# Kernel tuning notes

Measured on AMD Instinct MI355X. Metric: run time of the kernel, lower is better.

## Reference

```python
import jax, jax.numpy as jnp
from jax import lax
import numpy as np

VOCAB, EMB, HID, ENC, ATT, P = 10000, 512, 1024, 2048, 512, 196
B, T = 64, 160
PAD_IDX = 3

def setup_inputs() -> dict:
    key = jax.random.key(0)
    ks = jax.random.split(key, 20)
    s = 0.02
    emb = jax.random.normal(ks[0], (VOCAB, EMB), jnp.float32) * s
    emb = emb.at[PAD_IDX].set(0.0)
    return {
        'image_embedding': jax.random.normal(ks[1], (B, P, ENC), jnp.float32),
        'padded_sentence': jax.random.randint(ks[2], (B, T), 0, VOCAB),
        'enc_h': jax.random.normal(ks[3], (2, B, HID // 2), jnp.float32),
        'enc_c': jax.random.normal(ks[4], (2, B, HID // 2), jnp.float32),
        'sentence_lens': jax.random.randint(ks[5], (B,), 1, T + 1),
        'emb': emb,
        'Wea': jax.random.normal(ks[6], (ATT, ENC), jnp.float32) * s,
        'bea': jnp.zeros((ATT,), jnp.float32),
        'Wda': jax.random.normal(ks[7], (ATT, HID), jnp.float32) * s,
        'bda': jnp.zeros((ATT,), jnp.float32),
        'wfa': jax.random.normal(ks[8], (ATT,), jnp.float32) * s,
        'bfa': jnp.zeros((), jnp.float32),
        'Wfb': jax.random.normal(ks[9], (ENC, HID), jnp.float32) * s,
        'bfb': jnp.zeros((ENC,), jnp.float32),
        'Wih': jax.random.normal(ks[10], (4 * HID, EMB + ENC), jnp.float32) * s,
        'bih': jnp.zeros((4 * HID,), jnp.float32),
        'Whh': jax.random.normal(ks[11], (4 * HID, HID), jnp.float32) * s,
        'bhh': jnp.zeros((4 * HID,), jnp.float32),
    }


def reference(image_embedding, padded_sentence, enc_h, enc_c, sentence_lens,
              emb, Wea, bea, Wda, bda, wfa, bfa, Wfb, bfb, Wih, bih, Whh, bhh):
    Tn = padded_sentence.shape[1]
    # sort by descending length (replicates sentence_lens.sort(descending=True))
    idx = jnp.argsort(-sentence_lens)
    img = image_embedding[idx]                   # [B,P,E]
    sent = padded_sentence[idx]                  # [B,T]
    lens = sentence_lens[idx]                    # [B]
    h0 = jnp.concatenate([enc_h[-2], enc_h[-1]], axis=1)[idx]  # [B,HID]
    c0 = jnp.concatenate([enc_c[-2], enc_c[-1]], axis=1)[idx]
    emb_eff = emb.at[PAD_IDX].set(0.0)           # padding_idx=3
    x_emb = emb_eff[sent]                        # [B,T,EMB]
    # encoder projection is h-independent: hoist out of the scan
    att1 = jnp.einsum('bpe,ae->bpa', img, Wea) + bea  # [B,P,ATT]

    def step(carry, xt):
        h, c = carry
        x_t, t = xt
        active = (t < lens)[:, None]             # ragged mask
        att2 = h @ Wda.T + bda                   # [B,ATT]
        e = jax.nn.relu(att1 + att2[:, None, :]) @ wfa + bfa  # [B,P]
        alpha = jax.nn.softmax(e, axis=1)
        context = jnp.einsum('bp,bpe->be', alpha, img)        # [B,ENC]
        gate = jax.nn.sigmoid(h @ Wfb.T + bfb)
        inp = jnp.concatenate([x_t, gate * context], axis=1)  # [B,EMB+ENC]
        gates = inp @ Wih.T + bih + h @ Whh.T + bhh           # [B,4*HID]
        i, f, g, o = jnp.split(gates, 4, axis=1)
        c_new = jax.nn.sigmoid(f) * c + jax.nn.sigmoid(i) * jnp.tanh(g)
        h_new = jax.nn.sigmoid(o) * jnp.tanh(c_new)
        h = jnp.where(active, h_new, h)
        c = jnp.where(active, c_new, c)
        out_t = jnp.where(active, h_new, 0.0)
        alpha_t = jnp.where(active, alpha, 0.0)
        return (h, c), (out_t, alpha_t)

    (_, _), (outs, alphas) = lax.scan(
        step, (h0, c0), (jnp.swapaxes(x_emb, 0, 1), jnp.arange(Tn)))
    outputs = jnp.swapaxes(outs, 0, 1)           # [B,T,HID]
    alphas = jnp.swapaxes(alphas, 0, 1)          # [B,T,P]
    # replicate the original's final reindex (outputs[ordered_idx], not inverse)
    return outputs[idx], alphas[idx]
```

## Files before the change

### kernel.cpp

```cpp
#include <hip/hip_runtime.h>
#include <hip/hip_bf16.h>
#include <math.h>

#define B 64
#define T 160
#define P 196
#define ENC 2048
#define ATT 512
#define EMB 512
#define HID 1024
#define KTOT 3584
#define N2 2560
#define KT4 112
#define NTHR 1024
#define NBLK 256
#define NGRP 16
#define GRPSZ (NBLK/NGRP)

typedef __attribute__((ext_vector_type(8))) short bf16x8;
typedef __attribute__((ext_vector_type(4))) float f32x4;
typedef float __attribute__((ext_vector_type(4))) vf4;

__device__ __forceinline__ float sigm(float x){ return 1.0f/(1.0f+__expf(-x)); }
__device__ __forceinline__ float bfu(short s){ return __uint_as_float(((unsigned)(unsigned short)s) << 16); }

__device__ __forceinline__ float ldgf(const float* p){ return *(const volatile float*)p; }
__device__ __forceinline__ void stgf(float* p, float v){ *(volatile float*)p = v; }
__device__ __forceinline__ void stgu(unsigned* p, unsigned v){ *(volatile unsigned*)p = v; }
__device__ __forceinline__ unsigned pkbf(float a, float b){
    unsigned ua = (unsigned)__bfloat16_as_ushort(__float2bfloat16(a));
    unsigned ub = (unsigned)__bfloat16_as_ushort(__float2bfloat16(b));
    return ua | (ub << 16);
}

__device__ __forceinline__ void gbar_arrive(unsigned* bar, unsigned k){
    asm volatile("s_waitcnt vmcnt(0)" ::: "memory");
    __syncthreads();
    if (threadIdx.x == 0){
        unsigned g = blockIdx.x & (NGRP-1);
        unsigned old = __hip_atomic_fetch_add(bar + g*256, 1u, __ATOMIC_RELAXED, __HIP_MEMORY_SCOPE_AGENT);
        if (old == (k + 1u)*GRPSZ - 1u){
            __hip_atomic_fetch_add(bar + NGRP*256, 1u, __ATOMIC_RELAXED, __HIP_MEMORY_SCOPE_AGENT);
        }
    }
}
__device__ __forceinline__ void gbar_wait(unsigned* bar, unsigned k){
    if (threadIdx.x == 0){
        unsigned b = blockIdx.x;
        if (b < NGRP){
            volatile unsigned* top = bar + NGRP*256;
            while (*top < (k + 1u)*NGRP) __builtin_amdgcn_s_sleep(2);
            *(volatile unsigned*)(bar + (NGRP + 1 + b)*256) = k + 1u;
        } else {
            volatile unsigned* rel = bar + (NGRP + 1 + (b & (NGRP-1)))*256;
            while (*rel < k + 1u) __builtin_amdgcn_s_sleep(2);
        }
    }
    __syncthreads();
    asm volatile("" ::: "memory");
}
__device__ __forceinline__ void gbar(unsigned* bar, unsigned k){
    gbar_arrive(bar, k);
    gbar_wait(bar, k);
}

__global__ void k_sort(const int* lens, int* idx, int* rank, unsigned* barCnt, int* nAct){
    __shared__ int L[B];
    int i = threadIdx.x;
    L[i] = lens[i];
    if (i < 33) barCnt[i*256] = 0u;
    __syncthreads();
    int li = L[i];
    int r = 0;
    for (int j = 0; j < B; ++j){
        int lj = L[j];
        if (lj > li || (lj == li && j < i)) r++;
    }
    rank[i] = r;
    idx[r] = i;
    for (int tt = i; tt < T; tt += B){
        int c = 0;
        for (int j = 0; j < B; ++j) c += (L[j] > tt) ? 1 : 0;
        nAct[tt] = c;
    }
}

__global__ void k_init_hc(const float* enc_h, const float* enc_c, const int* idx,
                          float* h, float* c, __hip_bfloat16* hbR0){
    int j = blockIdx.x;
    int o = idx[j];
    for (int k = threadIdx.x; k < HID; k += blockDim.x){
        float hv = (k < 512) ? enc_h[o*512 + k] : enc_h[B*512 + o*512 + (k-512)];
        float cv = (k < 512) ? enc_c[o*512 + k] : enc_c[B*512 + o*512 + (k-512)];
        h[j*HID + k] = hv;
        c[j*HID + k] = cv;
        hbR0[j*HID + k] = __float2bfloat16(hv);
    }
}

__global__ void k_cvt_wcat(const float* Wih, const float* Whh, __hip_bfloat16* Wfrag){
    size_t i = (size_t)blockIdx.x*256 + threadIdx.x;
    int e = (int)(i & 7);
    size_t t2 = i >> 3;
    int lane = (int)(t2 & 63);
    size_t t3 = t2 >> 6;
    int kt = (int)(t3 % KT4);
    int strip = (int)(t3 / KT4);
    int n = strip*16 + (lane & 15);
    int r = (n & 3)*HID + (n >> 2);
    int k = kt*32 + (lane >> 4)*8 + e;
    float v = (k < EMB+ENC) ? Wih[(size_t)r*(EMB+ENC) + k]
                            : Whh[(size_t)r*HID + (k - EMB - ENC)];
    Wfrag[i] = __float2bfloat16(v);
}

__global__ void k_bsum(const float* bih, const float* bhh, float* bsum){
    int n = blockIdx.x*256 + threadIdx.x;
    int r = (n & 3)*HID + (n >> 2);
    bsum[n] = bih[r] + bhh[r];
}

__global__ void k_cvt_w2(const float* Wda, const float* bda, const float* Wfb, const float* bfb,
                         __hip_bfloat16* W2, float* bias2){
    int n = blockIdx.x;
    const float* src = (n < ATT) ? (Wda + (size_t)n*HID) : (Wfb + (size_t)(n-ATT)*HID);
    __hip_bfloat16* dst = W2 + (size_t)n*HID;
    for (int k = threadIdx.x; k < HID; k += 256) dst[k] = __float2bfloat16(src[k]);
    if (threadIdx.x == 0) bias2[n] = (n < ATT) ? bda[n] : bfb[n-ATT];
}

__global__ void k_cvt_emb(const float* emb, __hip_bfloat16* emb_bf){
    size_t i = (size_t)blockIdx.x*256 + threadIdx.x;
    emb_bf[i] = __float2bfloat16(emb[i]);
}

__global__ void k_cvt_wea(const float* Wea, __hip_bfloat16* Wea_bf){
    int n = blockIdx.x;
    for (int k = threadIdx.x; k < ENC; k += 256)
        Wea_bf[(size_t)n*ENC + k] = __float2bfloat16(Wea[(size_t)n*ENC + k]);
}

__global__ void k_cvt_img(const float* img, const int* idx, __hip_bfloat16* img_s){
    int j = blockIdx.y;
    int o = idx[j];
    size_t off = (size_t)blockIdx.x*256 + threadIdx.x;
    img_s[(size_t)j*P*ENC + off] = __float2bfloat16(img[(size_t)o*P*ENC + off]);
}

__global__ __launch_bounds__(256) void k_att1m(const __hip_bfloat16* img_s, const __hip_bfloat16* Wea_bf,
                                               const float* bea, __hip_bfloat16* att1w){
    int m0 = blockIdx.x * 64, n0 = blockIdx.y * 64;
    int tid = threadIdx.x, w = tid >> 6, l = tid & 63, lm = l & 15, lk = l >> 4;
    const short* ap = (const short*)img_s + (size_t)(m0 + 16*w + lm)*ENC + 8*lk;
    const short* bp = (const short*)Wea_bf + (size_t)(n0 + lm)*ENC + 8*lk;
    f32x4 acc[4];
    #pragma unroll
    for (int nt=0; nt<4; ++nt) acc[nt] = (f32x4){0.f,0.f,0.f,0.f};
    #pragma unroll 4
    for (int kt = 0; kt < ENC/32; ++kt){
        bf16x8 a = *(const bf16x8*)(ap + kt*32);
        #pragma unroll
        for (int nt=0; nt<4; ++nt){
            bf16x8 bb = *(const bf16x8*)(bp + (size_t)nt*16*ENC + kt*32);
            acc[nt] = __builtin_amdgcn_mfma_f32_16x16x32_bf16(a, bb, acc[nt], 0,0,0);
        }
    }
    #pragma unroll
    for (int nt=0; nt<4; ++nt){
        int n = n0 + nt*16 + lm;
        float bv = bea[n];
        #pragma unroll
        for (int r=0; r<4; ++r){
            int m = m0 + 16*w + 4*lk + r;
            att1w[(size_t)m*ATT + n] = __float2bfloat16(acc[nt][r] + bv);
        }
    }
}

struct SP {
    const __hip_bfloat16 *att1w, *img_s, *emb_bf, *Wfrag, *W2;
    const float *bsum, *bias2, *wfa, *bfa;
    const int *sent, *idx, *rank, *lens, *nAct;
    float *D2;
    __hip_bfloat16 *gcR, *hbR;
    float *hF0, *hF1, *cW;
    float *outH, *outA;
    unsigned *barCnt;
};

__global__ __launch_bounds__(1024, 4) void k_scan(SP p){
    __shared__ short WcatL[KT4*64*8];
    __shared__ union {
        struct { float Dp[4][64][17]; float hS[64][4]; int tokL[64], lensL[64], wLs[64]; } gem;
        struct { float att2L[512]; float wfaL[512]; float red[1024]; float aL[208]; float ctxP[8][512]; } p23;
    } sh;

    int b = blockIdx.x, tid = threadIdx.x;
    int w = tid >> 6, l = tid & 63, lm = l & 15, lk = l >> 4;
    unsigned bk = 0;

    {
        const bf16x8* src = (const bf16x8*)((const short*)p.Wfrag + (size_t)b*KT4*64*8);
        bf16x8* dst = (bf16x8*)WcatL;
        #pragma unroll
        for (int i = 0; i < KT4*64/NTHR; ++i) dst[tid + i*NTHR] = src[tid + i*NTHR];
    }
    __syncthreads();

    float bfa0 = p.bfa[0];

    for (int t = 0; t < T; ++t){
        const __hip_bfloat16* hbIn = p.hbR + (size_t)t*B*HID;
        __hip_bfloat16*       hbOut = p.hbR + (size_t)(t+1)*B*HID;
        const __hip_bfloat16* gcT  = p.gcR + (size_t)t*B*ENC;
        const float* hFIn = (t & 1) ? p.hF1 : p.hF0;
        float*       hFOut = (t & 1) ? p.hF0 : p.hF1;
        int nAct = p.nAct[t];

        if (b < N2/16){
            int n0 = b*16;
            int rt = w & 3, kq = w >> 2;
            if (16*rt < nAct){
                const short* ap = (const short*)hbIn + (size_t)(16*rt + lm)*HID + kq*256 + 8*lk;
                const short* bp = (const short*)p.W2 + (size_t)(n0 + lm)*HID + kq*256 + 8*lk;
                f32x4 acc = {0.f,0.f,0.f,0.f};
                #pragma unroll
                for (int kt = 0; kt < 8; ++kt){
                    bf16x8 a = *(const bf16x8*)(ap + kt*32);
                    bf16x8 bb = *(const bf16x8*)(bp + kt*32);
                    acc = __builtin_amdgcn_mfma_f32_16x16x32_bf16(a, bb, acc, 0,0,0);
                }
                #pragma unroll
                for (int r=0; r<4; ++r) sh.gem.Dp[kq][16*rt + 4*lk + r][lm] = acc[r];
            }
            __syncthreads();
            int m = tid >> 4, nl = tid & 15;
            if (m < nAct){
                stgf(&p.D2[m*N2 + n0 + nl],
                     sh.gem.Dp[0][m][nl] + sh.gem.Dp[1][m][nl]
                   + sh.gem.Dp[2][m][nl] + sh.gem.Dp[3][m][nl] + p.bias2[n0 + nl]);
            }
        }
        gbar(p.barCnt, bk); bk++;

        int jj = b & 63, qq = b >> 6;
        int oo = p.idx[jj], wjj = p.rank[jj], ljj = p.lens[oo];
        {
            if (t < ljj){
                if (tid < 512){
                    sh.p23.att2L[tid] = ldgf(&p.D2[jj*N2 + tid]);
                    sh.p23.wfaL[tid]  = p.wfa[tid];
                }
                __syncthreads();

                int pp = tid & 255, ah = tid >> 8;
                float acc = 0.f;
                if (pp < P){
                    const short* ar = (const short*)p.att1w + (size_t)(jj*P + pp)*ATT + ah*128;
                    #pragma unroll 8
                    for (int k8 = 0; k8 < 16; ++k8){
                        bf16x8 v = *(const bf16x8*)(ar + k8*8);
                        #pragma unroll
                        for (int z=0; z<8; ++z){
                            int a = ah*128 + k8*8 + z;
                            acc += fmaxf(bfu(v[z]) + sh.p23.att2L[a], 0.f) * sh.p23.wfaL[a];
                        }
                    }
                }
                sh.p23.red[tid] = acc;
                __syncthreads();
                float e = -1e30f;
                if (tid < P) e = sh.p23.red[tid] + sh.p23.red[tid+256] + sh.p23.red[tid+512] + sh.p23.red[tid+768] + bfa0;
                __syncthreads();
                sh.p23.red[tid] = (tid < P) ? e : -1e30f;
                __syncthreads();
                for (int s = 512; s > 0; s >>= 1){
                    if (tid < s) sh.p23.red[tid] = fmaxf(sh.p23.red[tid], sh.p23.red[tid+s]);
                    __syncthreads();
                }
                float m = sh.p23.red[0];
                __syncthreads();
                float ex = (tid < P) ? __expf(e - m) : 0.f;
                sh.p23.red[tid] = ex;
                __syncthreads();
                for (int s = 512; s > 0; s >>= 1){
                    if (tid < s) sh.p23.red[tid] += sh.p23.red[tid+s];
                    __syncthreads();
                }
                float ssum = sh.p23.red[0];
                if (tid < P) sh.p23.aL[tid] = ex / ssum;
                if (tid >= P && tid < 208) sh.p23.aL[tid] = 0.f;
                __syncthreads();

                const short* ib = (const short*)p.img_s + (size_t)jj*P*ENC + qq*512 + l*8;
                float a8[8];
                #pragma unroll
                for (int z=0; z<8; ++z) a8[z] = 0.f;
                #pragma unroll 4
                for (int i = 0; i < 13; ++i){
                    int pp2 = w + 16*i;
                    int pr = (pp2 < P) ? pp2 : 0;
                    bf16x8 v = *(const bf16x8*)(ib + (size_t)pr*ENC);
                    float al = sh.p23.aL[pp2];
                    #pragma unroll
                    for (int z=0; z<8; ++z) a8[z] += al * bfu(v[z]);
                }
                if (w < 8){
                    #pragma unroll
                    for (int z=0; z<8; ++z) sh.p23.ctxP[w][l*8+z] = a8[z];
                }
                __syncthreads();
                if (w >= 8){
                    #pragma unroll
                    for (int z=0; z<8; ++z) sh.p23.ctxP[w-8][l*8+z] += a8[z];
                }
                __syncthreads();
                if (tid < 256){
                    int d0 = 2*tid;
                    float c0 = 0.f, c1 = 0.f;
                    #pragma unroll
                    for (int r=0; r<8; ++r){ c0 += sh.p23.ctxP[r][d0]; c1 += sh.p23.ctxP[r][d0+1]; }
                    int eg0 = qq*512 + d0;
                    float g0 = sigm(ldgf(&p.D2[jj*N2 + ATT + eg0]));
                    float g1 = sigm(ldgf(&p.D2[jj*N2 + ATT + eg0 + 1]));
                    stgu((unsigned*)((short*)gcT + jj*ENC + eg0), pkbf(g0*c0, g1*c1));
                }
            }
        }
        gbar_arrive(p.barCnt, bk);

        if (qq == 0 && tid < P){
            float av = (t < ljj) ? sh.p23.aL[tid] : 0.f;
            p.outA[((size_t)(wjj*T + t))*P + tid] = av;
        }
        __syncthreads();

        if (tid < 64){
            int o = p.idx[tid];
            sh.gem.tokL[tid] = p.sent[o*T + t];
            sh.gem.lensL[tid] = p.lens[o];
            sh.gem.wLs[tid] = p.rank[tid];
        }
        __syncthreads();
        {
            int rt = w & 3, kq = w >> 2;
            bool act = (16*rt < nAct);
            int mrow = 16*rt + lm;
            f32x4 acc = {0.f,0.f,0.f,0.f};
            const short* aEmb = 0; const short* aGc = 0; const short* aH = 0;
            const bf16x8* BL = (const bf16x8*)WcatL;
            if (act){
                int tok = sh.gem.tokL[mrow];
                aEmb = (const short*)p.emb_bf + (size_t)tok*EMB + 8*lk;
                aGc  = (const short*)gcT + (size_t)mrow*ENC + 8*lk;
                aH   = (const short*)hbIn + (size_t)mrow*HID + 8*lk;
                if (kq == 0){
                    #pragma unroll 8
                    for (int kt = 0; kt < 16; ++kt){
                        bf16x8 a = *(const bf16x8*)(aEmb + kt*32);
                        acc = __builtin_amdgcn_mfma_f32_16x16x32_bf16(a, BL[kt*64 + l], acc, 0,0,0);
                    }
                } else if (kq == 2){
                    #pragma unroll
                    for (int kt = 80; kt < 84; ++kt){
                        bf16x8 a = *(const bf16x8*)(aH + (kt-80)*32);
                        acc = __builtin_amdgcn_mfma_f32_16x16x32_bf16(a, BL[kt*64 + l], acc, 0,0,0);
                    }
                } else if (kq == 3){
                    #pragma unroll 7
                    for (int kt = 84; kt < 112; ++kt){
                        bf16x8 a = *(const bf16x8*)(aH + (kt-80)*32);
                        acc = __builtin_amdgcn_mfma_f32_16x16x32_bf16(a, BL[kt*64 + l], acc, 0,0,0);
                    }
                }
            }
            gbar_wait(p.barCnt, bk); bk++;

            if (act){
                if (kq == 0){
                    #pragma unroll 6
                    for (int kt = 16; kt < 28; ++kt){
                        bf16x8 a = *(const bf16x8*)(aGc + (kt-16)*32);
                        acc = __builtin_amdgcn_mfma_f32_16x16x32_bf16(a, BL[kt*64 + l], acc, 0,0,0);
                    }
                } else if (kq == 1){
                    #pragma unroll 7
                    for (int kt = 28; kt < 56; ++kt){
                        bf16x8 a = *(const bf16x8*)(aGc + (kt-16)*32);
                        acc = __builtin_amdgcn_mfma_f32_16x16x32_bf16(a, BL[kt*64 + l], acc, 0,0,0);
                    }
                } else if (kq == 2){
                    #pragma unroll 6
                    for (int kt = 56; kt < 80; ++kt){
                        bf16x8 a = *(const bf16x8*)(aGc + (kt-16)*32);
                        acc = __builtin_amdgcn_mfma_f32_16x16x32_bf16(a, BL[kt*64 + l], acc, 0,0,0);
                    }
                }
                #pragma unroll
                for (int r=0; r<4; ++r) sh.gem.Dp[kq][16*rt + 4*lk + r][lm] = acc[r];
            }
        }
        __syncthreads();

        int j2 = tid & 63, du = tid >> 6;
        int u = 4*b + du;
        float cNew = 0.f, hNew = 0.f, hKeep = 0.f, cOld = 0.f;
        bool active = false;
        if (tid < 256){
            float g4[4];
            #pragma unroll
            for (int g=0; g<4; ++g){
                int nl = 4*du + g;
                g4[g] = sh.gem.Dp[0][j2][nl] + sh.gem.Dp[1][j2][nl]
                      + sh.gem.Dp[2][j2][nl] + sh.gem.Dp[3][j2][nl] + p.bsum[16*b + nl];
            }
            float ig = sigm(g4[0]), fg = sigm(g4[1]), gg = tanhf(g4[2]), og = sigm(g4[3]);
            cOld = p.cW[j2*HID + u];
            cNew = fg*cOld + ig*gg;
            hNew = og*tanhf(cNew);
            active = (t < sh.gem.lensL[j2]);
            float hOld = hFIn[j2*HID + u];
            hKeep = active ? hNew : hOld;
            sh.gem.hS[j2][du] = hKeep;
        }
        __syncthreads();
        if (tid < 128){
            int jb = tid & 63, dp = tid >> 6;
            int u0 = 4*b + 2*dp;
            stgu((unsigned*)((short*)hbOut + jb*HID + u0),
                 pkbf(sh.gem.hS[jb][2*dp], sh.gem.hS[jb][2*dp+1]));
        }
        gbar_arrive(p.barCnt, bk);
        if (tid < 256){
            p.cW[j2*HID + u] = active ? cNew : cOld;
            hFOut[j2*HID + u] = hKeep;
            p.outH[((size_t)sh.gem.wLs[j2]*T + t)*HID + u] = active ? hNew : 0.f;
        }
        gbar_wait(p.barCnt, bk); bk++;
    }
}

extern "C" void kernel_launch(void* const* d_in, const int* in_sizes, int n_in,
                              void* d_out, int out_size, void* d_ws, size_t ws_size,
                              hipStream_t stream) {
    const float* img   = (const float*)d_in[0];
    const int*   sent  = (const int*)  d_in[1];
    const float* enc_h = (const float*)d_in[2];
    const float* enc_c = (const float*)d_in[3];
    const int*   lens  = (const int*)  d_in[4];
    const float* emb   = (const float*)d_in[5];
    const float* Wea   = (const float*)d_in[6];
    const float* bea   = (const float*)d_in[7];
    const float* Wda   = (const float*)d_in[8];
    const float* bda   = (const float*)d_in[9];
    const float* wfa   = (const float*)d_in[10];
    const float* bfa   = (const float*)d_in[11];
    const float* Wfb   = (const float*)d_in[12];
    const float* bfb   = (const float*)d_in[13];
    const float* Wih   = (const float*)d_in[14];
    const float* bih   = (const float*)d_in[15];
    const float* Whh   = (const float*)d_in[16];
    const float* bhh   = (const float*)d_in[17];

    float* outH = (float*)d_out;
    float* outA = outH + (size_t)B*T*HID;

    char* wsb = (char*)d_ws;
    size_t off = 0;
    int* idxW  = (int*)(wsb + off); off += 256;
    int* rankW = (int*)(wsb + off); off += 256;
    int* nActW = (int*)(wsb + off); off += 1024;
    unsigned* barCnt = (unsigned*)(wsb + off); off += 36864;
    __hip_bfloat16* att1w = (__hip_bfloat16*)(wsb + off); off += (size_t)B*P*ATT*2;
    __hip_bfloat16* img_s = (__hip_bfloat16*)(wsb + off); off += (size_t)B*P*ENC*2;
    __hip_bfloat16* emb_bf= (__hip_bfloat16*)(wsb + off); off += (size_t)10000*EMB*2;
    __hip_bfloat16* Wfrag = (__hip_bfloat16*)(wsb + off); off += (size_t)4*HID*KTOT*2;
    __hip_bfloat16* W2    = (__hip_bfloat16*)(wsb + off); off += (size_t)N2*HID*2;
    __hip_bfloat16* Wea_bf= (__hip_bfloat16*)(wsb + off); off += (size_t)ATT*ENC*2;
    float* bsum  = (float*)(wsb + off); off += 4*HID*4;
    float* bias2 = (float*)(wsb + off); off += N2*4;
    float* hA    = (float*)(wsb + off); off += B*HID*4;
    float* hB    = (float*)(wsb + off); off += B*HID*4;
    float* cWs   = (float*)(wsb + off); off += B*HID*4;
    float* D2    = (float*)(wsb + off); off += (size_t)B*N2*4;
    __hip_bfloat16* gcR = (__hip_bfloat16*)(wsb + off); off += (size_t)T*B*ENC*2;
    __hip_bfloat16* hbR = (__hip_bfloat16*)(wsb + off); off += (size_t)(T+1)*B*HID*2;

    k_sort<<<1, 64, 0, stream>>>(lens, idxW, rankW, barCnt, nActW);
    k_init_hc<<<B, 256, 0, stream>>>(enc_h, enc_c, idxW, hA, cWs, hbR);
    k_cvt_wcat<<<57344, 256, 0, stream>>>(Wih, Whh, Wfrag);
    k_bsum<<<16, 256, 0, stream>>>(bih, bhh, bsum);
    k_cvt_w2<<<N2, 256, 0, stream>>>(Wda, bda, Wfb, bfb, W2, bias2);
    k_cvt_emb<<<20000, 256, 0, stream>>>(emb, emb_bf);
    k_cvt_wea<<<ATT, 256, 0, stream>>>(Wea, Wea_bf);
    k_cvt_img<<<dim3(P*ENC/256, B), 256, 0, stream>>>(img, idxW, img_s);
    k_att1m<<<dim3((B*P)/64, ATT/64), 256, 0, stream>>>(img_s, Wea_bf, bea, att1w);

    SP sp;
    sp.att1w = att1w; sp.img_s = img_s; sp.emb_bf = emb_bf; sp.Wfrag = Wfrag; sp.W2 = W2;
    sp.bsum = bsum; sp.bias2 = bias2; sp.wfa = wfa; sp.bfa = bfa;
    sp.sent = sent; sp.idx = idxW; sp.rank = rankW; sp.lens = lens; sp.nAct = nActW;
    sp.D2 = D2; sp.gcR = gcR; sp.hbR = hbR;
    sp.hF0 = hA; sp.hF1 = hB; sp.cW = cWs;
    sp.outH = outH; sp.outA = outA;
    sp.barCnt = barCnt;

    void* args[] = { &sp };
    hipLaunchCooperativeKernel(reinterpret_cast<void*>(k_scan), dim3(NBLK), dim3(NTHR),
                               args, 0, stream);
}
```

Before: 7.031 ms.

## Replace atomic-counter grid barrier with per-block flag slots and wave-parallel polling

The hierarchical grid barrier used by the persistent recurrent kernel no longer uses atomic fetch-add counters. Each block now writes its epoch to its own padded flag slot. Sixteen leader blocks each poll their group's arrival flags in parallel with a wavefront vote, then exchange group-done flags and publish a release flag that the other blocks spin on. The aim is to shorten each of the many per-timestep barriers by removing atomic serialization. The cost is a larger barrier workspace and more polling traffic from the leader wavefronts.

```diff
diff --git a/kernel.cpp b/kernel.cpp
--- a/kernel.cpp
+++ b/kernel.cpp
@@ -17,6 +17,10 @@
 #define NGRP 16
 #define GRPSZ (NBLK/NGRP)
 
+#define ARR_W 0
+#define GD_W  16384
+#define REL_W 17408
+
 typedef __attribute__((ext_vector_type(8))) short bf16x8;
 typedef __attribute__((ext_vector_type(4))) float f32x4;
 typedef float __attribute__((ext_vector_type(4))) vf4;
@@ -36,24 +40,24 @@
 __device__ __forceinline__ void gbar_arrive(unsigned* bar, unsigned k){
     asm volatile("s_waitcnt vmcnt(0)" ::: "memory");
     __syncthreads();
-    if (threadIdx.x == 0){
-        unsigned g = blockIdx.x & (NGRP-1);
-        unsigned old = __hip_atomic_fetch_add(bar + g*256, 1u, __ATOMIC_RELAXED, __HIP_MEMORY_SCOPE_AGENT);
-        if (old == (k + 1u)*GRPSZ - 1u){
-            __hip_atomic_fetch_add(bar + NGRP*256, 1u, __ATOMIC_RELAXED, __HIP_MEMORY_SCOPE_AGENT);
-        }
-    }
+    if (threadIdx.x == 0)
+        *(volatile unsigned*)(bar + ARR_W + (unsigned)blockIdx.x*64) = k + 1u;
 }
 __device__ __forceinline__ void gbar_wait(unsigned* bar, unsigned k){
-    if (threadIdx.x == 0){
-        unsigned b = blockIdx.x;
-        if (b < NGRP){
-            volatile unsigned* top = bar + NGRP*256;
-            while (*top < (k + 1u)*NGRP) __builtin_amdgcn_s_sleep(2);
-            *(volatile unsigned*)(bar + (NGRP + 1 + b)*256) = k + 1u;
-        } else {
-            volatile unsigned* rel = bar + (NGRP + 1 + (b & (NGRP-1)))*256;
-            while (*rel < k + 1u) __builtin_amdgcn_s_sleep(2);
+    int b = blockIdx.x, tid = threadIdx.x;
+    if (b < NGRP){
+        if (tid < 64){
+            volatile unsigned* s = (volatile unsigned*)(bar + ARR_W + (unsigned)((tid & 15)*NGRP + b)*64);
+            while (!__all(*s >= k + 1u)) __builtin_amdgcn_s_sleep(1);
+            if (tid == 0) *(volatile unsigned*)(bar + GD_W + b*64) = k + 1u;
+            volatile unsigned* g = (volatile unsigned*)(bar + GD_W + (tid & 15)*64);
+            while (!__all(*g >= k + 1u)) __builtin_amdgcn_s_sleep(1);
+            if (tid == 0) *(volatile unsigned*)(bar + REL_W + b*64) = k + 1u;
+        }
+    } else {
+        if (tid == 0){
+            volatile unsigned* r = (volatile unsigned*)(bar + REL_W + (b & (NGRP-1))*64);
+            while (*r < k + 1u) __builtin_amdgcn_s_sleep(1);
         }
     }
     __syncthreads();
@@ -68,7 +72,12 @@
     __shared__ int L[B];
     int i = threadIdx.x;
     L[i] = lens[i];
-    if (i < 33) barCnt[i*256] = 0u;
+    for (int s = i; s < 288; s += B){
+        int wofs = (s < 256) ? (ARR_W + s*64)
+                 : (s < 272) ? (GD_W + (s-256)*64)
+                             : (REL_W + (s-272)*64);
+        barCnt[wofs] = 0u;
+    }
     __syncthreads();
     int li = L[i];
     int r = 0;
@@ -470,7 +479,7 @@
     int* idxW  = (int*)(wsb + off); off += 256;
     int* rankW = (int*)(wsb + off); off += 256;
     int* nActW = (int*)(wsb + off); off += 1024;
-    unsigned* barCnt = (unsigned*)(wsb + off); off += 36864;
+    unsigned* barCnt = (unsigned*)(wsb + off); off += 131072;
     __hip_bfloat16* att1w = (__hip_bfloat16*)(wsb + off); off += (size_t)B*P*ATT*2;
     __hip_bfloat16* img_s = (__hip_bfloat16*)(wsb + off); off += (size_t)B*P*ENC*2;
     __hip_bfloat16* emb_bf= (__hip_bfloat16*)(wsb + off); off += (size_t)10000*EMB*2;
```

Measured after the change: 7.047 ms (median of 2 runs). About the same (+0.2%).
